# Optimization experiments

Measured on AMD Instinct MI355X. Metric: run time of the kernel, lower is better.

## Reference

```python
import jax, jax.numpy as jnp
import numpy as np

B, N, C, H, NL, NH = 8, 1024, 256, 512, 3, 8


def setup_inputs() -> dict:
    key = jax.random.key(0)
    ks = jax.random.split(key, 16)
    g = lambda k, shape: jax.random.normal(k, shape, jnp.float32) * 0.02
    return dict(
        concept_features=jax.random.normal(ks[0], (B, N, C), jnp.float32),
        adjacency_matrix=jax.random.uniform(ks[1], (B, N, N), jnp.float32),
        edge_types=jax.random.randint(ks[2], (B, N, N), 0, 10),
        concept_mask=jnp.ones((B, N), bool),
        W_emb=g(ks[3], (H, C)), b_emb=jnp.zeros((H,), jnp.float32),
        W_in=g(ks[4], (NL, 3 * H, H)), b_in=jnp.zeros((NL, 3 * H), jnp.float32),
        W_out=g(ks[5], (NL, H, H)), b_out=jnp.zeros((NL, H), jnp.float32),
        W_conv=g(ks[6], (NL, H, H)), b_conv=jnp.zeros((NL, H), jnp.float32),
        W_cls=g(ks[7], (1, H)), b_cls=jnp.zeros((1,), jnp.float32),
        W_diff=g(ks[8], (5, H)), b_diff=jnp.zeros((5,), jnp.float32),
        W_pre=g(ks[9], (1, 2 * H)), b_pre=jnp.zeros((1,), jnp.float32),
        W_pool=g(ks[10], (H, H)), b_pool=jnp.zeros((H,), jnp.float32),
    )


def reference(concept_features, adjacency_matrix, edge_types, concept_mask,
              W_emb, b_emb, W_in, b_in, W_out, b_out, W_conv, b_conv,
              W_cls, b_cls, W_diff, b_diff, W_pre, b_pre, W_pool, b_pool):
    Bq, Nc, _ = concept_features.shape
    Hd = W_emb.shape[0]
    dh = Hd // NH

    def mha(x, Wi, bi, Wo, bo):
        # torch nn.MultiheadAttention with batch_first=False: the (B,N,H)
        # input is treated as (seq=B, batch=N, embed=H) -> attention over B.
        qkv = x @ Wi.T + bi                      # (B,N,3H)
        q, k, v = jnp.split(qkv, 3, axis=-1)
        rs = lambda t: t.reshape(Bq, Nc, NH, dh)
        q, k, v = rs(q), rs(k), rs(v)
        sc = jnp.einsum('inhd,jnhd->nhij', q, k) / jnp.sqrt(jnp.float32(dh))
        a = jax.nn.softmax(sc, axis=-1)          # (N,NH,B,B)
        o = jnp.einsum('nhij,jnhd->inhd', a, v).reshape(Bq, Nc, Hd)
        return o @ Wo.T + bo

    def ln(x):  # F.layer_norm, no affine
        m = x.mean(-1, keepdims=True)
        v = ((x - m) ** 2).mean(-1, keepdims=True)
        return (x - m) * jax.lax.rsqrt(v + 1e-5)

    x = concept_features @ W_emb.T + b_emb       # (B,N,H)
    for l in range(W_in.shape[0]):
        att = mha(x, W_in[l], b_in[l], W_out[l], b_out[l])
        conv = att @ W_conv[l].T + b_conv[l]
        agg = jnp.einsum('bij,bjh->bih', adjacency_matrix, conv)
        x = ln(x + agg)

    mastery = x @ W_cls.T + b_cls                # (B,N,1)
    diff = x @ W_diff.T + b_diff                 # (B,N,5)

    # O(N^2) pairwise loop -> bilinear decomposition:
    # score(i,j) = x_i @ W_pre[:, :H].T + x_j @ W_pre[:, H:].T + b
    h1 = (x @ W_pre[:, :Hd].T)[..., 0]           # (B,N)
    h2 = (x @ W_pre[:, Hd:].T)[..., 0]           # (B,N)
    pair = h1[:, :, None] + h2[:, None, :] + b_pre[0]  # (B,N,N)
    off = ~np.eye(Nc, dtype=bool).reshape(-1)    # static mask, i!=j row-major
    prereq = pair.reshape(Bq, Nc * Nc)[:, off][..., None]  # (B,N*(N-1),1)

    graph = x.mean(axis=1) @ W_pool.T + b_pool   # (B,H)
    return (x, mastery, diff, prereq, graph)
```

## Files before the change

kernel.cpp:

```cpp
#include <hip/hip_runtime.h>
#include <hip/hip_bf16.h>

typedef unsigned short ushort_t;
typedef __attribute__((ext_vector_type(4))) float floatx4;
typedef __attribute__((ext_vector_type(8))) __bf16 bf16x8;
typedef __attribute__((ext_vector_type(4))) unsigned short ushortx4;
typedef __attribute__((ext_vector_type(8))) unsigned short ushortx8;

static __device__ __forceinline__ float b2f(ushort_t u) {
  union { unsigned int i; float f; } v; v.i = ((unsigned int)u) << 16; return v.f;
}
static __device__ __forceinline__ ushort_t f2b(float f) {
  unsigned int x = __float_as_uint(f);
  unsigned int r = (x + 0x7fffu + ((x >> 16) & 1u)) >> 16;
  return (ushort_t)r;
}
static __device__ __forceinline__ void glds16(const ushort_t* g, ushort_t* l) {
  __builtin_amdgcn_global_load_lds(
      (const __attribute__((address_space(1))) unsigned int*)g,
      (__attribute__((address_space(3))) unsigned int*)l, 16, 0, 0);
}

template<int MODE>
static __device__ __forceinline__ void gemm_core(
    const ushort_t* __restrict__ Ab, const ushort_t* __restrict__ Bm,
    const float* __restrict__ bias,
    ushort_t* __restrict__ outB, ushort_t* __restrict__ C1,
    int N, int K, int m0, int n0, int kbeg, int kend,
    ushort_t* As, ushort_t* Bs)
{
  const int tid  = threadIdx.x;
  const int wid  = tid >> 6;
  const int lane = tid & 63;
  const int quad = lane >> 4;
  const int l16  = lane & 15;

  const int wr = (wid >> 1) * 64;
  const int wc = (wid & 1) * 64;

  const int srow = tid >> 3;
  const int scj  = ((tid & 7) ^ (srow & 7)) * 8;
  const long abase = (long)(m0 + srow) * K + scj;
  const long bbase = (long)(n0 + srow) * K + scj;

  floatx4 acc[4][4];
#pragma unroll
  for (int i = 0; i < 4; ++i)
#pragma unroll
    for (int j = 0; j < 4; ++j) acc[i][j] = (floatx4){0.f, 0.f, 0.f, 0.f};

  const int rx = l16 & 7;

  for (int k0 = kbeg; k0 < kend; k0 += 64) {
    __syncthreads();
#pragma unroll
    for (int p = 0; p < 4; ++p)
      glds16(Ab + abase + 32 * p * (long)K + k0, &As[tid * 8 + p * 2048]);
#pragma unroll
    for (int p = 0; p < 4; ++p)
      glds16(Bm + bbase + 32 * p * (long)K + k0, &Bs[tid * 8 + p * 2048]);
    __syncthreads();

#pragma unroll
    for (int kk = 0; kk < 2; ++kk) {
      bf16x8 a[4], b[4];
#pragma unroll
      for (int i = 0; i < 4; ++i)
        a[i] = *(const bf16x8*)(&As[(wr + i * 16 + l16) * 64 +
                                    (((kk * 4 + quad) ^ rx) << 3)]);
#pragma unroll
      for (int j = 0; j < 4; ++j)
        b[j] = *(const bf16x8*)(&Bs[(wc + j * 16 + l16) * 64 +
                                    (((kk * 4 + quad) ^ rx) << 3)]);
#pragma unroll
      for (int i = 0; i < 4; ++i)
#pragma unroll
        for (int j = 0; j < 4; ++j)
          acc[i][j] = __builtin_amdgcn_mfma_f32_16x16x32_bf16(a[i], b[j], acc[i][j], 0, 0, 0);
    }
  }

#pragma unroll
  for (int j = 0; j < 4; ++j) {
    int col = n0 + wc + j * 16 + l16;
    float bv = (bias != nullptr) ? bias[col] : 0.f;
#pragma unroll
    for (int i = 0; i < 4; ++i) {
      int mbase = m0 + wr + i * 16 + quad * 4;
      if constexpr (MODE == 1) {
#pragma unroll
        for (int r = 0; r < 4; ++r)
          outB[(long)(mbase + r) * N + col] = f2b(acc[i][j][r] + bv);
      } else if constexpr (MODE == 2) {
        int b = mbase >> 10, jrow = mbase & 1023;
        ushortx4 pk;
#pragma unroll
        for (int r = 0; r < 4; ++r) pk[r] = f2b(acc[i][j][r] + bv);
        *(ushortx4*)(outB + ((long)b * N + col) * 1024 + jrow) = pk;
      } else {
        ushort_t* o = (n0 < 512) ? outB : C1;
        const int cw = (n0 < 512) ? 512 : 1536;
        const int cc = (n0 < 512) ? col : col - 512;
#pragma unroll
        for (int r = 0; r < 4; ++r)
          o[(long)(mbase + r) * cw + cc] = f2b(acc[i][j][r] + bv);
      }
    }
  }
}

template<int MODE, int KS>
__global__ __launch_bounds__(256, 3) void gemm_bt(
    const ushort_t* __restrict__ Ab, const ushort_t* __restrict__ Bm,
    const float* __restrict__ bias,
    ushort_t* __restrict__ C0, ushort_t* __restrict__ C1,
    int N, int K, long aBatch, long bBatch, long cBatch)
{
  __shared__ __align__(16) ushort_t As[128 * 64];
  __shared__ __align__(16) ushort_t Bs[128 * 64];
  const int lin = blockIdx.y * gridDim.x + blockIdx.x;
  const int m0 = (lin % gridDim.y) * 128;
  const int n0 = (lin / gridDim.y) * 128;
  const int z  = (KS > 1) ? (int)(blockIdx.z / KS) : blockIdx.z;
  const int kq = (KS > 1) ? (int)(blockIdx.z % KS) : 0;
  const int kbeg = kq * (K / KS);
  const int kend = kbeg + (K / KS);
  ushort_t* outB = (KS >= 2 && kq == 1) ? C1 : C0;
  gemm_core<MODE>(Ab + (long)z * aBatch, Bm + (long)z * bBatch, bias,
                  outB + ((MODE == 1) ? (long)z * cBatch : 0), C1,
                  N, K, m0, n0, kbeg, kend, As, Bs);
}

__global__ __launch_bounds__(256, 3) void setup_gemm(
    const ushort_t* __restrict__ Wcb, const ushort_t* __restrict__ WoT,
    ushort_t* __restrict__ Wfb,
    const ushort_t* __restrict__ Winb, const ushort_t* __restrict__ WembT,
    ushort_t* __restrict__ Wq0t)
{
  __shared__ __align__(16) ushort_t As[128 * 64];
  __shared__ __align__(16) ushort_t Bs[128 * 64];
  const int lin = blockIdx.x;
  const int z = blockIdx.z;
  if (z < 3) {
    if (lin >= 16) return;
    const long off = (long)z * 262144;
    gemm_core<1>(Wcb + off, WoT + off, nullptr, Wfb + off, nullptr,
                 512, 512, (lin & 3) * 128, (lin >> 2) * 128, 0, 512, As, Bs);
  } else {
    gemm_core<1>(Winb, WembT, nullptr, Wq0t, nullptr,
                 256, 512, (lin % 12) * 128, (lin / 12) * 128, 0, 512, As, Bs);
  }
}

__global__ __launch_bounds__(256) void prep_kernel(
    const float* __restrict__ Win,  ushort_t* __restrict__ Winb,
    const float* __restrict__ Wemb, ushort_t* __restrict__ Wq0,
    const float* __restrict__ Wconv, ushort_t* __restrict__ Wcb,
    const float* __restrict__ ADJ,  ushort_t* __restrict__ ADJb,
    const float* __restrict__ CF,   ushort_t* __restrict__ CFb,
    const float* __restrict__ Wout, ushort_t* __restrict__ WoT,
    const float* __restrict__ bout, const float* __restrict__ bconv,
    float* __restrict__ bfused,
    ushort_t* __restrict__ WembT,
    const float* __restrict__ bemb, const float* __restrict__ bin0,
    float* __restrict__ bcat,
    const float* __restrict__ Wpool, float* __restrict__ WpT)
{
  __shared__ float tile[64][65];
  const int bid = blockIdx.x, tid = threadIdx.x;
  if (bid < 6720) {
    const float* src; ushort_t* dst; long i;
    if (bid < 1152)      { src = Win;   dst = Winb; i = (long)bid * 256 + tid; }
    else if (bid < 1216) { src = Wemb;  dst = Wq0;  i = (long)(bid - 1152) * 256 + tid; }
    else if (bid < 1600) { src = Wconv; dst = Wcb;  i = (long)(bid - 1216) * 256 + tid; }
    else if (bid < 5696) { src = ADJ;   dst = ADJb; i = (long)(bid - 1600) * 256 + tid; }
    else                 { src = CF;    dst = CFb;  i = (long)(bid - 5696) * 256 + tid; }
    floatx4 a = ((const floatx4*)src)[2 * i];
    floatx4 b = ((const floatx4*)src)[2 * i + 1];
    ushortx4 ha, hb;
#pragma unroll
    for (int r = 0; r < 4; ++r) { ha[r] = f2b(a[r]); hb[r] = f2b(b[r]); }
    ((ushortx4*)dst)[2 * i] = ha; ((ushortx4*)dst)[2 * i + 1] = hb;
  } else if (bid < 6912) {
    const int t = bid - 6720;
    const int z = t >> 6, k0 = ((t >> 3) & 7) * 64, j0 = (t & 7) * 64;
    const long base = (long)z * 262144;
#pragma unroll
    for (int p = 0; p < 16; ++p) {
      int idx = tid + p * 256;
      int jj = idx >> 6, kk = idx & 63;
      tile[jj][kk] = Wout[base + (long)(j0 + jj) * 512 + k0 + kk];
    }
    __syncthreads();
#pragma unroll
    for (int p = 0; p < 16; ++p) {
      int idx = tid + p * 256;
      int kk = idx >> 6, jj = idx & 63;
      WoT[base + (long)(k0 + kk) * 512 + j0 + jj] = f2b(tile[jj][kk]);
    }
  } else if (bid < 6944) {
    const int t = bid - 6912;
    const int j0 = (t >> 2) * 64, k0 = (t & 3) * 64;
#pragma unroll
    for (int p = 0; p < 16; ++p) {
      int idx = tid + p * 256;
      int jj = idx >> 6, kk = idx & 63;
      tile[jj][kk] = Wemb[(long)(j0 + jj) * 256 + k0 + kk];
    }
    __syncthreads();
#pragma unroll
    for (int p = 0; p < 16; ++p) {
      int idx = tid + p * 256;
      int kk = idx >> 6, jj = idx & 63;
      WembT[(long)(k0 + kk) * 512 + j0 + jj] = f2b(tile[jj][kk]);
    }
  } else if (bid < 7328) {
    const int w = tid >> 6, lane = tid & 63;
    const int gi = (bid - 6944) * 4 + w;
    const int l = gi >> 9, o = gi & 511;
    float p = 0.f;
#pragma unroll
    for (int k = 0; k < 8; ++k)
      p += Wconv[(long)l * 262144 + (long)o * 512 + lane + 64 * k] *
           bout[l * 512 + lane + 64 * k];
#pragma unroll
    for (int msk = 1; msk <= 32; msk <<= 1) p += __shfl_xor(p, msk);
    if (lane == 0) bfused[gi] = p + bconv[l * 512 + o];
  } else if (bid < 7712) {
    const int w = tid >> 6, lane = tid & 63;
    const int o = (bid - 7328) * 4 + w;
    float p = 0.f;
#pragma unroll
    for (int k = 0; k < 8; ++k)
      p += Win[(long)o * 512 + lane + 64 * k] * bemb[lane + 64 * k];
#pragma unroll
    for (int msk = 1; msk <= 32; msk <<= 1) p += __shfl_xor(p, msk);
    if (lane == 0) bcat[512 + o] = p + bin0[o];
  } else if (bid < 7714) {
    int idx = (bid - 7712) * 256 + tid;
    bcat[idx] = bemb[idx];
  } else {
    const int t = bid - 7714;
    const int j0 = (t >> 3) * 64, k0 = (t & 7) * 64;
#pragma unroll
    for (int p = 0; p < 16; ++p) {
      int idx = tid + p * 256;
      int jj = idx >> 6, kk = idx & 63;
      tile[jj][kk] = Wpool[(long)(j0 + jj) * 512 + k0 + kk];
    }
    __syncthreads();
#pragma unroll
    for (int p = 0; p < 16; ++p) {
      int idx = tid + p * 256;
      int kk = idx >> 6, jj = idx & 63;
      WpT[(long)(k0 + kk) * 512 + j0 + jj] = tile[jj][kk];
    }
  }
}

__global__ __launch_bounds__(512, 8) void attn_kernel(
    const ushort_t* __restrict__ qkv, ushort_t* __restrict__ outp)
{
  __shared__ ushort_t qs[8 * 1544];
  __shared__ float aw[8][64];
  const int tid = threadIdx.x;
  const int n = blockIdx.x;

  const ushort_t* src = qkv + (long)n * 1536;
#pragma unroll
  for (int p = 0; p < 3; ++p) {
    int c = tid + p * 512;
    int i = c / 192, off = (c % 192) * 8;
    *(ushortx8*)(&qs[i * 1544 + off]) =
        *(const ushortx8*)(src + (long)i * 1024 * 1536 + off);
  }
  __syncthreads();

  const int h    = tid >> 6;
  const int lane = tid & 63;
  const int i = lane >> 3, j = lane & 7;
  const ushort_t* qrow = &qs[i * 1544 + h * 64];
  const ushort_t* krow = &qs[j * 1544 + 512 + h * 64];
  float s = 0.f;
#pragma unroll
  for (int c8 = 0; c8 < 8; ++c8) {
    ushortx8 qa = *(const ushortx8*)(qrow + c8 * 8);
    ushortx8 ka = *(const ushortx8*)(krow + c8 * 8);
#pragma unroll
    for (int r = 0; r < 8; ++r) s += b2f(qa[r]) * b2f(ka[r]);
  }
  s *= 0.125f;

  float m = s;
  m = fmaxf(m, __shfl_xor(m, 1));
  m = fmaxf(m, __shfl_xor(m, 2));
  m = fmaxf(m, __shfl_xor(m, 4));
  float e = __expf(s - m);
  float sum = e;
  sum += __shfl_xor(sum, 1);
  sum += __shfl_xor(sum, 2);
  sum += __shfl_xor(sum, 4);
  aw[h][lane] = e / sum;

  float vv[8];
#pragma unroll
  for (int jj = 0; jj < 8; ++jj)
    vv[jj] = b2f(qs[jj * 1544 + 1024 + h * 64 + lane]);
  const long ob = (long)n * 512 + h * 64 + lane;
#pragma unroll
  for (int ii = 0; ii < 8; ++ii) {
    float acc = 0.f;
#pragma unroll
    for (int jj = 0; jj < 8; ++jj) acc += aw[h][ii * 8 + jj] * vv[jj];
    outp[ob + (long)ii * 1024 * 512] = f2b(acc);
  }
}

__global__ __launch_bounds__(256) void ln_kernel(
    const ushort_t* __restrict__ xb,
    const ushort_t* __restrict__ aggA, const ushort_t* __restrict__ aggB,
    ushort_t* __restrict__ outB)
{
  const int w = threadIdx.x >> 6, lane = threadIdx.x & 63;
  const long base = ((long)blockIdx.x * 4 + w) * 512;
  float v[8];
  float s = 0.f;
#pragma unroll
  for (int k = 0; k < 8; ++k) {
    long idx = base + lane + 64 * k;
    v[k] = b2f(xb[idx]) + b2f(aggA[idx]) + b2f(aggB[idx]);
    s += v[k];
  }
#pragma unroll
  for (int msk = 1; msk <= 32; msk <<= 1) s += __shfl_xor(s, msk);
  float mean = s * (1.f / 512.f);
  float vv = 0.f;
#pragma unroll
  for (int k = 0; k < 8; ++k) { float d = v[k] - mean; vv += d * d; }
#pragma unroll
  for (int msk = 1; msk <= 32; msk <<= 1) vv += __shfl_xor(vv, msk);
  float inv = rsqrtf(vv * (1.f / 512.f) + 1e-5f);
#pragma unroll
  for (int k = 0; k < 8; ++k)
    outB[base + lane + 64 * k] = f2b((v[k] - mean) * inv);
}

__global__ __launch_bounds__(256) void final_ln_heads_kernel(
    const ushort_t* __restrict__ xb,
    const ushort_t* __restrict__ aggA, const ushort_t* __restrict__ aggB,
    float* __restrict__ out_x,
    const float* __restrict__ Wcls, const float* __restrict__ bcls,
    const float* __restrict__ Wdiff, const float* __restrict__ bdiff,
    const float* __restrict__ Wpre,
    float* __restrict__ mastery, float* __restrict__ diff,
    float* __restrict__ h1, float* __restrict__ h2,
    float* __restrict__ xp)
{
  __shared__ float sp4[4][512];
  const int w = threadIdx.x >> 6, lane = threadIdx.x & 63;
  const long row = (long)blockIdx.x * 4 + w;
  const long base = row * 512;
  float v[8];
  float s = 0.f;
#pragma unroll
  for (int k = 0; k < 8; ++k) {
    long idx = base + lane + 64 * k;
    v[k] = b2f(xb[idx]) + b2f(aggA[idx]) + b2f(aggB[idx]);
    s += v[k];
  }
#pragma unroll
  for (int msk = 1; msk <= 32; msk <<= 1) s += __shfl_xor(s, msk);
  float mean = s * (1.f / 512.f);
  float vv = 0.f;
#pragma unroll
  for (int k = 0; k < 8; ++k) { float d = v[k] - mean; vv += d * d; }
#pragma unroll
  for (int msk = 1; msk <= 32; msk <<= 1) vv += __shfl_xor(vv, msk);
  float inv = rsqrtf(vv * (1.f / 512.f) + 1e-5f);
#pragma unroll
  for (int k = 0; k < 8; ++k) {
    v[k] = (v[k] - mean) * inv;
    out_x[base + lane + 64 * k] = v[k];
    sp4[w][lane + 64 * k] = v[k];
  }
  __syncthreads();
  for (int t = threadIdx.x; t < 512; t += 256)
    xp[(long)blockIdx.x * 512 + t] =
        sp4[0][t] + sp4[1][t] + sp4[2][t] + sp4[3][t];
#pragma unroll
  for (int o = 0; o < 8; ++o) {
    const float* wp = (o == 0) ? Wcls
                    : (o <= 5) ? (Wdiff + (o - 1) * 512)
                    : (o == 6) ? Wpre : (Wpre + 512);
    float p = 0.f;
#pragma unroll
    for (int k = 0; k < 8; ++k) p += v[k] * wp[lane + 64 * k];
#pragma unroll
    for (int msk = 1; msk <= 32; msk <<= 1) p += __shfl_xor(p, msk);
    if (lane == 0) {
      if (o == 0)      mastery[row] = p + bcls[0];
      else if (o <= 5) diff[row * 5 + (o - 1)] = p + bdiff[o - 1];
      else if (o == 6) h1[row] = p;
      else             h2[row] = p;
    }
  }
}

__global__ __launch_bounds__(256) void epi_kernel(
    const float* __restrict__ h1, const float* __restrict__ h2,
    const float* __restrict__ bpre, float* __restrict__ outp,
    const float* __restrict__ xp, float* __restrict__ xq)
{
  const int bid = blockIdx.x;
  if (bid < 8184) {
    const int g = bid * 256 + threadIdx.x;
    const int t = g * 4;
    const int b = t / 1047552;
    const int r = t - b * 1047552;
    const float bp = bpre[0];
    const float* h1b = h1 + b * 1024;
    const float* h2b = h2 + b * 1024;
    floatx4 o;
#pragma unroll
    for (int k = 0; k < 4; ++k) {
      int rk = r + k;
      int i = rk / 1023;
      int pos = rk - i * 1023;
      int j = pos + (pos >= i);
      o[k] = h1b[i] + bp + h2b[j];
    }
    *(floatx4*)(outp + t) = o;
  } else {
    const int q0 = bid - 8184;
    const float* p = xp + (long)q0 * 32 * 512;
#pragma unroll
    for (int cc = 0; cc < 2; ++cc) {
      int c = threadIdx.x + cc * 256;
      float s = 0.f;
#pragma unroll
      for (int q = 0; q < 32; ++q) s += p[q * 512 + c];
      xq[(long)q0 * 512 + c] = s;
    }
  }
}

__global__ __launch_bounds__(256) void graph_kernel(
    const float* __restrict__ xq, const float* __restrict__ WpT,
    const float* __restrict__ bpool, float* __restrict__ g)
{
  __shared__ float xms[512];
  const int b = blockIdx.x;
  const float* xb = xq + (long)b * 8 * 512;
#pragma unroll
  for (int cc = 0; cc < 2; ++cc) {
    int c = threadIdx.x + cc * 256;
    float s = 0.f;
#pragma unroll
    for (int p = 0; p < 8; ++p) s += xb[p * 512 + c];
    xms[c] = s;
  }
  __syncthreads();
#pragma unroll
  for (int oo = 0; oo < 2; ++oo) {
    int o = threadIdx.x + oo * 256;
    float acc = 0.f;
    for (int h = 0; h < 512; ++h) acc += xms[h] * WpT[h * 512 + o];
    g[b * 512 + o] = acc * (1.f / 1024.f) + bpool[o];
  }
}

extern "C" void kernel_launch(void* const* d_in, const int* in_sizes, int n_in,
                              void* d_out, int out_size, void* d_ws, size_t ws_size,
                              hipStream_t stream)
{
  const float* CF    = (const float*)d_in[0];
  const float* ADJ   = (const float*)d_in[1];
  const float* Wemb  = (const float*)d_in[4];
  const float* bemb  = (const float*)d_in[5];
  const float* Win   = (const float*)d_in[6];
  const float* bin   = (const float*)d_in[7];
  const float* Wout  = (const float*)d_in[8];
  const float* bout  = (const float*)d_in[9];
  const float* Wconv = (const float*)d_in[10];
  const float* bconv = (const float*)d_in[11];
  const float* Wcls  = (const float*)d_in[12];
  const float* bcls  = (const float*)d_in[13];
  const float* Wdiff = (const float*)d_in[14];
  const float* bdiff = (const float*)d_in[15];
  const float* Wpre  = (const float*)d_in[16];
  const float* bpre  = (const float*)d_in[17];
  const float* Wpool = (const float*)d_in[18];
  const float* bpool = (const float*)d_in[19];

  ushort_t* W = (ushort_t*)d_ws;
  ushort_t* xb   = W;
  ushort_t* qkvb = W + 4194304;
  ushort_t* cT    = qkvb;
  ushort_t* aggA  = qkvb + 4194304;
  ushort_t* aggB  = qkvb + 8388608;
  ushort_t* WoT   = qkvb + 4194304;
  ushort_t* Wcb   = qkvb + 4980736;
  ushort_t* WembT = qkvb + 5767168;
  ushort_t* Winb = W + 16777216;
  ushort_t* Wfb  = W + 19136512;
  ushort_t* ADJb = W + 19922944;
  ushort_t* CFb  = W + 28311552;
  ushort_t* Wq0  = W + 32505856;
  float* bfused = (float*)(W + 33030144);
  float* bcat   = bfused + 1536;
  float* h1     = bcat + 2048;
  float* h2     = h1 + 8192;
  float* xp     = h2 + 8192;
  float* xq     = xp + 1048576;
  float* WpT    = xq + 32768;

  float* out_x       = (float*)d_out;
  float* out_mastery = out_x + 4194304;
  float* out_diff    = out_mastery + 8192;
  float* out_prereq  = out_diff + 40960;
  float* out_graph   = out_prereq + 8380416;
  ushort_t* aob = (ushort_t*)out_x;

  dim3 blk(256);

  prep_kernel<<<dim3(7778), blk, 0, stream>>>(
      Win, Winb, Wemb, Wq0, Wconv, Wcb, ADJ, ADJb, CF, CFb,
      Wout, WoT, bout, bconv, bfused, WembT, bemb, bin, bcat,
      Wpool, WpT);
  setup_gemm<<<dim3(24, 1, 4), blk, 0, stream>>>(
      Wcb, WoT, Wfb, Winb, WembT, Wq0 + 512 * 256);

  for (int l = 0; l < 3; ++l) {
    if (l == 0) {
      gemm_bt<3, 1><<<dim3(16, 64, 1), blk, 0, stream>>>(
          CFb, Wq0, bcat, xb, qkvb, 2048, 256, 0, 0, 0);
    } else {
      gemm_bt<1, 1><<<dim3(12, 64, 1), blk, 0, stream>>>(
          xb, Winb + (long)l * 786432, bin + l * 1536,
          qkvb, nullptr, 1536, 512, 0, 0, 0);
    }
    attn_kernel<<<dim3(1024), dim3(512), 0, stream>>>(qkvb, aob);
    gemm_bt<2, 1><<<dim3(4, 64, 1), blk, 0, stream>>>(
        aob, Wfb + (long)l * 262144, bfused + l * 512,
        cT, nullptr, 512, 512, 0, 0, 0);
    gemm_bt<1, 2><<<dim3(4, 8, 16), blk, 0, stream>>>(
        ADJb, cT, nullptr, aggA, aggB,
        512, 1024, 1048576, 524288, 524288);
    if (l < 2)
      ln_kernel<<<dim3(2048), blk, 0, stream>>>(xb, aggA, aggB, xb);
    else
      final_ln_heads_kernel<<<dim3(2048), blk, 0, stream>>>(
          xb, aggA, aggB, out_x, Wcls, bcls, Wdiff, bdiff, Wpre,
          out_mastery, out_diff, h1, h2, xp);
  }

  epi_kernel<<<dim3(8248), blk, 0, stream>>>(h1, h2, bpre, out_prereq,
                                             xp, xq);
  graph_kernel<<<dim3(8), blk, 0, stream>>>(xq, WpT, bpool, out_graph);
}
```

Baseline: 423.3 us.

## Add 256x256-tile 8-wave double-buffered GEMM for QKV projections

Introduces a new GEMM kernel with 512 threads, 256x256 output tiles, double-buffered LDS staged through global_load_lds, XOR-swizzled LDS layout, interleaved prefetch and setprio around MFMA bursts. It replaces the 128x128 gemm_bt for the layer-0 embedding+QKV GEMM and the later QKV projections. The aim is more operand reuse per LDS load and overlap of global loads with MFMA work. Grids shrink to 256 and 192 blocks, so fewer than one wave of blocks covers the 256 CUs, which risks underusing the GPU; the larger LDS footprint and accumulator register count also limit occupancy.

```diff
diff --git a/kernel.cpp b/kernel.cpp
--- a/kernel.cpp
+++ b/kernel.cpp
@@ -19,6 +19,140 @@
   __builtin_amdgcn_global_load_lds(
       (const __attribute__((address_space(1))) unsigned int*)g,
       (__attribute__((address_space(3))) unsigned int*)l, 16, 0, 0);
+}
+
+template<int MODE>
+__global__ __launch_bounds__(512, 2) void gemm8p(
+    const ushort_t* __restrict__ Ab, const ushort_t* __restrict__ Bm,
+    const float* __restrict__ bias,
+    ushort_t* __restrict__ C0, ushort_t* __restrict__ C1,
+    int N, int K)
+{
+  __shared__ __align__(16) ushort_t As[2 * 16384];
+  __shared__ __align__(16) ushort_t Bs[2 * 16384];
+  const int tid  = threadIdx.x;
+  const int wid  = tid >> 6;
+  const int lane = tid & 63;
+  const int quad = lane >> 4;
+  const int l16  = lane & 15;
+  const int rx   = l16 & 7;
+  const int lin = blockIdx.y * gridDim.x + blockIdx.x;
+  const int m0 = (lin % gridDim.y) * 256;
+  const int n0 = (lin / gridDim.y) * 256;
+  const int NT = K >> 6;
+
+  const int srow = tid >> 3;
+  const int scj  = ((tid & 7) ^ (srow & 7)) * 8;
+  const long abase = (long)(m0 + srow) * K + scj;
+  const long bbase = (long)(n0 + srow) * K + scj;
+
+  floatx4 acc[16][2];
+#pragma unroll
+  for (int i = 0; i < 16; ++i) {
+    acc[i][0] = (floatx4){0.f, 0.f, 0.f, 0.f};
+    acc[i][1] = (floatx4){0.f, 0.f, 0.f, 0.f};
+  }
+
+#define STG_A(bf, h, t) do { const long k0_ = (long)(t) << 6; \
+    glds16(Ab + abase + (long)((h) * 128     ) * K + k0_, &As[(bf) * 16384 + (h) * 8192 + tid * 8]); \
+    glds16(Ab + abase + (long)((h) * 128 + 64) * K + k0_, &As[(bf) * 16384 + (h) * 8192 + 4096 + tid * 8]); } while (0)
+#define STG_B(bf, h, t) do { const long k0_ = (long)(t) << 6; \
+    glds16(Bm + bbase + (long)((h) * 128     ) * K + k0_, &Bs[(bf) * 16384 + (h) * 8192 + tid * 8]); \
+    glds16(Bm + bbase + (long)((h) * 128 + 64) * K + k0_, &Bs[(bf) * 16384 + (h) * 8192 + 4096 + tid * 8]); } while (0)
+
+  STG_A(0, 0, 0); STG_B(0, 0, 0); STG_B(0, 1, 0); STG_A(0, 1, 0);
+
+  for (int t = 0; t < NT; ++t) {
+    const int c = t & 1;
+    const ushort_t* AsC = &As[c * 16384];
+    const ushort_t* BsC = &Bs[c * 16384];
+    const bool pf = (t + 1 < NT);
+    bf16x8 a[8];
+    bf16x8 bfr[2][2];
+
+    asm volatile("s_waitcnt vmcnt(2)" ::: "memory");
+    __builtin_amdgcn_s_barrier();
+#pragma unroll
+    for (int j = 0; j < 2; ++j)
+#pragma unroll
+      for (int kc = 0; kc < 2; ++kc)
+        bfr[j][kc] = *(const bf16x8*)(&BsC[(wid * 32 + j * 16 + l16) * 64 +
+                                           (((kc * 4 + quad) ^ rx) << 3)]);
+#pragma unroll
+    for (int f = 0; f < 8; ++f)
+      a[f] = *(const bf16x8*)(&AsC[(f * 16 + l16) * 64 + ((quad ^ rx) << 3)]);
+    if (pf) STG_A(c ^ 1, 0, t + 1);
+    __builtin_amdgcn_s_setprio(1);
+#pragma unroll
+    for (int f = 0; f < 8; ++f) {
+      acc[f][0] = __builtin_amdgcn_mfma_f32_16x16x32_bf16(a[f], bfr[0][0], acc[f][0], 0, 0, 0);
+      acc[f][1] = __builtin_amdgcn_mfma_f32_16x16x32_bf16(a[f], bfr[1][0], acc[f][1], 0, 0, 0);
+    }
+    __builtin_amdgcn_s_setprio(0);
+
+#pragma unroll
+    for (int f = 0; f < 8; ++f)
+      a[f] = *(const bf16x8*)(&AsC[(f * 16 + l16) * 64 + (((4 + quad) ^ rx) << 3)]);
+    if (pf) STG_B(c ^ 1, 0, t + 1);
+    __builtin_amdgcn_s_setprio(1);
+#pragma unroll
+    for (int f = 0; f < 8; ++f) {
+      acc[f][0] = __builtin_amdgcn_mfma_f32_16x16x32_bf16(a[f], bfr[0][1], acc[f][0], 0, 0, 0);
+      acc[f][1] = __builtin_amdgcn_mfma_f32_16x16x32_bf16(a[f], bfr[1][1], acc[f][1], 0, 0, 0);
+    }
+    __builtin_amdgcn_s_setprio(0);
+
+    if (pf) { asm volatile("s_waitcnt vmcnt(4)" ::: "memory"); }
+    else    { asm volatile("s_waitcnt vmcnt(0)" ::: "memory"); }
+    __builtin_amdgcn_s_barrier();
+#pragma unroll
+    for (int f = 0; f < 8; ++f)
+      a[f] = *(const bf16x8*)(&AsC[(128 + f * 16 + l16) * 64 + ((quad ^ rx) << 3)]);
+    if (pf) STG_B(c ^ 1, 1, t + 1);
+    __builtin_amdgcn_s_setprio(1);
+#pragma unroll
+    for (int f = 0; f < 8; ++f) {
+      acc[8 + f][0] = __builtin_amdgcn_mfma_f32_16x16x32_bf16(a[f], bfr[0][0], acc[8 + f][0], 0, 0, 0);
+      acc[8 + f][1] = __builtin_amdgcn_mfma_f32_16x16x32_bf16(a[f], bfr[1][0], acc[8 + f][1], 0, 0, 0);
+    }
+    __builtin_amdgcn_s_setprio(0);
+
+#pragma unroll
+    for (int f = 0; f < 8; ++f)
+      a[f] = *(const bf16x8*)(&AsC[(128 + f * 16 + l16) * 64 + (((4 + quad) ^ rx) << 3)]);
+    if (pf) STG_A(c ^ 1, 1, t + 1);
+    __builtin_amdgcn_s_setprio(1);
+#pragma unroll
+    for (int f = 0; f < 8; ++f) {
+      acc[8 + f][0] = __builtin_amdgcn_mfma_f32_16x16x32_bf16(a[f], bfr[0][1], acc[8 + f][0], 0, 0, 0);
+      acc[8 + f][1] = __builtin_amdgcn_mfma_f32_16x16x32_bf16(a[f], bfr[1][1], acc[8 + f][1], 0, 0, 0);
+    }
+    __builtin_amdgcn_s_setprio(0);
+  }
+#undef STG_A
+#undef STG_B
+
+#pragma unroll
+  for (int fj = 0; fj < 2; ++fj) {
+    int col = n0 + wid * 32 + fj * 16 + l16;
+    float bv = (bias != nullptr) ? bias[col] : 0.f;
+#pragma unroll
+    for (int fi = 0; fi < 16; ++fi) {
+      int mbase = m0 + fi * 16 + quad * 4;
+      if constexpr (MODE == 1) {
+#pragma unroll
+        for (int r = 0; r < 4; ++r)
+          C0[(long)(mbase + r) * N + col] = f2b(acc[fi][fj][r] + bv);
+      } else {
+        ushort_t* o = (n0 < 512) ? C0 : C1;
+        const int cw = (n0 < 512) ? 512 : 1536;
+        const int cc = (n0 < 512) ? col : col - 512;
+#pragma unroll
+        for (int r = 0; r < 4; ++r)
+          o[(long)(mbase + r) * cw + cc] = f2b(acc[fi][fj][r] + bv);
+      }
+    }
+  }
 }
 
 template<int MODE>
@@ -91,19 +225,12 @@
 #pragma unroll
         for (int r = 0; r < 4; ++r)
           outB[(long)(mbase + r) * N + col] = f2b(acc[i][j][r] + bv);
-      } else if constexpr (MODE == 2) {
+      } else {
         int b = mbase >> 10, jrow = mbase & 1023;
         ushortx4 pk;
 #pragma unroll
         for (int r = 0; r < 4; ++r) pk[r] = f2b(acc[i][j][r] + bv);
         *(ushortx4*)(outB + ((long)b * N + col) * 1024 + jrow) = pk;
-      } else {
-        ushort_t* o = (n0 < 512) ? outB : C1;
-        const int cw = (n0 < 512) ? 512 : 1536;
-        const int cc = (n0 < 512) ? col : col - 512;
-#pragma unroll
-        for (int r = 0; r < 4; ++r)
-          o[(long)(mbase + r) * cw + cc] = f2b(acc[i][j][r] + bv);
       }
     }
   }
@@ -522,6 +649,7 @@
   ushort_t* aob = (ushort_t*)out_x;
 
   dim3 blk(256);
+  dim3 blk8(512);
 
   prep_kernel<<<dim3(7778), blk, 0, stream>>>(
       Win, Winb, Wemb, Wq0, Wconv, Wcb, ADJ, ADJb, CF, CFb,
@@ -532,12 +660,12 @@
 
   for (int l = 0; l < 3; ++l) {
     if (l == 0) {
-      gemm_bt<3, 1><<<dim3(16, 64, 1), blk, 0, stream>>>(
-          CFb, Wq0, bcat, xb, qkvb, 2048, 256, 0, 0, 0);
+      gemm8p<3><<<dim3(8, 32), blk8, 0, stream>>>(
+          CFb, Wq0, bcat, xb, qkvb, 2048, 256);
     } else {
-      gemm_bt<1, 1><<<dim3(12, 64, 1), blk, 0, stream>>>(
+      gemm8p<1><<<dim3(6, 32), blk8, 0, stream>>>(
           xb, Winb + (long)l * 786432, bin + l * 1536,
-          qkvb, nullptr, 1536, 512, 0, 0, 0);
+          qkvb, nullptr, 1536, 512);
     }
     attn_kernel<<<dim3(1024), dim3(512), 0, stream>>>(qkvb, aob);
     gemm_bt<2, 1><<<dim3(4, 64, 1), blk, 0, stream>>>(
```

After: 420.8 us. Within noise of the previous version (-0.6%).
